# Kernel optimization log

Hardware: AMD Instinct MI355X
Metric: run time of the kernel (lower is better)

The kernel has to match this reference:

```python
import jax, jax.numpy as jnp
import numpy as np

WS = (17, 5, 1)
NT = 23  # 17+5+1 tokens across levels
TABLE_ROWS = (2 * WS[0] - 1) * (2 * WS[0] - 1)  # 1089


def _rel_index():
    cs = []
    for i, w in enumerate(WS):
        c = np.arange(w, dtype=np.float32) - w // 2
        if i < len(WS) - 1:
            c = c * WS[0] / w  # rescale coarser levels to finest grid
        cs.append(c)
    c = np.concatenate(cs)  # [23]
    return (c[:, None] - c[None, :]) + (WS[0] - 1)  # [23,23] float

REL_IDX = jnp.asarray(_rel_index())


def _avgpool1d(x):
    # AvgPool1d(kernel=2, stride=2, padding=1, count_include_pad=False) on last axis (odd L)
    return jnp.concatenate([x[..., :1], (x[..., 1::2] + x[..., 2::2]) * 0.5], axis=-1)


def _l2norm(x):
    n = jnp.linalg.norm(x, axis=-1, keepdims=True)
    return x / jnp.maximum(n, 1e-12)


def _pos_embed(table, abs_bias):
    # table [1089,H], abs_bias [3,H,1,1,1] -> [1,H,1,23,23]
    idx = REL_IDX.reshape(-1)
    fl = jnp.clip(jnp.floor(idx), 0, TABLE_ROWS - 1).astype(jnp.int32)
    ce = jnp.clip(jnp.ceil(idx), 0, TABLE_ROWS - 1).astype(jnp.int32)
    w_ce = (idx - fl.astype(idx.dtype))[:, None]
    pe = (1.0 - w_ce) * table[fl] + w_ce * table[ce]  # [529,H]
    H = table.shape[1]
    pe = pe.reshape(1, 1, NT, NT, H).transpose(0, 4, 1, 2, 3)  # [1,H,1,23,23]
    chunks = jnp.split(pe, [WS[0], WS[0] + WS[1]], axis=3)
    chunks = [c + abs_bias[i][None] for i, c in enumerate(chunks)]
    return jnp.concatenate(chunks, axis=-2)


def _hifi(xh0, xh1, xh2, h_table, h_abs, h_proj_w, h_proj_b):
    q = jnp.concatenate([xh0[0], xh1[0], xh2[0]], axis=-2)  # [B,Hh,hd,23,S]
    k = jnp.concatenate([xh0[1], xh1[1], xh2[1]], axis=-2)
    v = jnp.concatenate([xh0[2], xh1[2], xh2[2]], axis=-2)
    attn = jnp.einsum('bhdts,bhdus->bhdtu', _l2norm(q), _l2norm(k))
    attn = attn + _pos_embed(h_table, h_abs)
    attn = jax.nn.softmax(attn, axis=-1)
    out = jnp.einsum('bhdtu,bhdus->bhdts', attn, v)
    return out @ h_proj_w.T + h_proj_b


def _lofi(xl0, xl1, xl2, l_table, l_abs, l_proj_w, l_proj_b):
    q = jnp.concatenate([xl0[0], xl1[0], xl2[0]], axis=-2)  # [B,Hl,hd,23,S]
    kvs = []
    for i, x in enumerate((xl0, xl1, xl2)):
        kv = x[1:]  # [2,B,Hl,hd,t_i,S]
        if i != 2:  # pool token axis for the two finer levels
            kv = jnp.moveaxis(_avgpool1d(jnp.moveaxis(kv, -2, -1)), -1, -2)
        kvs.append(kv)
    kv = jnp.concatenate(kvs, axis=-2)  # [2,B,Hl,hd,13,S]
    k, v = kv[0], kv[1]
    attn = jnp.einsum('bhdts,bhdus->bhdtu', _l2norm(q), _l2norm(k))  # [B,Hl,hd,23,13]
    pe = _pos_embed(l_table, l_abs)  # [1,Hl,1,23,23]
    Hl = l_table.shape[1]
    p1 = _avgpool1d(pe[..., :WS[0]].reshape(Hl, NT, WS[0])).reshape(1, Hl, 1, NT, -1)
    p2 = _avgpool1d(pe[..., WS[0]:WS[0] + WS[1]].reshape(Hl, NT, WS[1])).reshape(1, Hl, 1, NT, -1)
    p3 = pe[..., -1:]
    attn = attn + jnp.concatenate([p1, p2, p3], axis=-1)
    attn = jax.nn.softmax(attn, axis=-1)
    out = jnp.einsum('bhdtu,bhdus->bhdts', attn, v)
    return out @ l_proj_w.T + l_proj_b


def _forward(xh0, xh1, xh2, xl0, xl1, xl2, h_table, h_abs, l_table, l_abs,
             h_proj_w, h_proj_b, l_proj_w, l_proj_b):
    h_out = _hifi(xh0, xh1, xh2, h_table, h_abs, h_proj_w, h_proj_b)  # [B,1,64,23,S]
    l_out = _lofi(xl0, xl1, xl2, l_table, l_abs, l_proj_w, l_proj_b)  # [B,3,64,23,S]
    return jnp.concatenate([h_out, l_out], axis=1)  # [B,4,64,23,S]


def setup_inputs() -> dict:
    key = jax.random.key(0)
    ks = jax.random.split(key, 14)
    B, hd, S = 4, 64, 1024
    Hh, Hl = 1, 3
    d = {
        'xh0': jax.random.normal(ks[0], (3, B, Hh, hd, 17, S), jnp.float32),
        'xh1': jax.random.normal(ks[1], (3, B, Hh, hd, 5, S), jnp.float32),
        'xh2': jax.random.normal(ks[2], (3, B, Hh, hd, 1, S), jnp.float32),
        'xl0': jax.random.normal(ks[3], (3, B, Hl, hd, 17, S), jnp.float32),
        'xl1': jax.random.normal(ks[4], (3, B, Hl, hd, 5, S), jnp.float32),
        'xl2': jax.random.normal(ks[5], (3, B, Hl, hd, 1, S), jnp.float32),
        'h_table': jax.random.normal(ks[6], (TABLE_ROWS, Hh), jnp.float32) * 0.02,
        'h_abs': jax.random.normal(ks[7], (3, Hh, 1, 1, 1), jnp.float32) * 0.02,
        'l_table': jax.random.normal(ks[8], (TABLE_ROWS, Hl), jnp.float32) * 0.02,
        'l_abs': jax.random.normal(ks[9], (3, Hl, 1, 1, 1), jnp.float32) * 0.02,
        'h_proj_w': jax.random.normal(ks[10], (S, S), jnp.float32) / np.sqrt(S),
        'h_proj_b': jax.random.normal(ks[11], (S,), jnp.float32) * 0.01,
        'l_proj_w': jax.random.normal(ks[12], (S, S), jnp.float32) / np.sqrt(S),
        'l_proj_b': jax.random.normal(ks[13], (S,), jnp.float32) * 0.01,
    }
    return d


def reference(xh0, xh1, xh2, xl0, xl1, xl2, h_table, h_abs, l_table, l_abs,
              h_proj_w, h_proj_b, l_proj_w, l_proj_b):
    return _forward(xh0, xh1, xh2, xl0, xl1, xl2, h_table, h_abs, l_table, l_abs,
                    h_proj_w, h_proj_b, l_proj_w, l_proj_b)
```

## Files before the change

### kernel.cpp

```cpp
#include <hip/hip_runtime.h>
#include <hip/hip_bf16.h>
#include <stdint.h>

#define DEV __device__ __forceinline__

typedef float f32x4 __attribute__((ext_vector_type(4)));
typedef __bf16 bf16x8 __attribute__((ext_vector_type(8)));

DEV __bf16 tobf(float x){
  union { __hip_bfloat16 s; __bf16 b; } u; u.s = __float2bfloat16(x); return u.b;
}
DEV float bflo(uint32_t u){ return __uint_as_float(u << 16); }
DEV float bfhi(uint32_t u){ return __uint_as_float(u & 0xffff0000u); }
DEV float dot4(const float4& a, const float4& b){
  return a.x*b.x + a.y*b.y + a.z*b.z + a.w*b.w;
}
DEV bf16x8 pack8(const float4& a, const float4& b){
  bf16x8 r;
  r[0]=tobf(a.x); r[1]=tobf(a.y); r[2]=tobf(a.z); r[3]=tobf(a.w);
  r[4]=tobf(b.x); r[5]=tobf(b.y); r[6]=tobf(b.z); r[7]=tobf(b.w);
  return r;
}
DEV uint32_t f2bf2(float x, float y){
  union { __hip_bfloat16 b[2]; uint32_t u; } cv;
  cv.b[0] = __float2bfloat16(x); cv.b[1] = __float2bfloat16(y);
  return cv.u;
}

DEV float relc(int j){
  if (j < 17) return (float)(j - 8);
  if (j < 22) return (float)(j - 19) * 3.4f;
  return 0.0f;
}
DEV int band_of(int t){ return t < 17 ? 0 : (t < 22 ? 1 : 2); }

template<int MODE> DEV void pool_map(int u, int& a, int& b){
  if (MODE == 0){ a = u; b = u; return; }
  if (u == 0){ a = 0; b = 0; }
  else if (u < 9){ a = 2*u - 1; b = 2*u; }
  else if (u == 9){ a = 17; b = 17; }
  else if (u < 12){ a = 2*u - 2; b = 2*u - 1; }
  else { a = 22; b = 22; }
}

DEV float interp_tab(const float* tab, int H, int h, int t, int u){
  float idx = relc(t) - relc(u) + 16.0f;
  float fl = floorf(idx);
  float ce = ceilf(idx);
  int fi = (int)fminf(fmaxf(fl, 0.f), 1088.f);
  int ci = (int)fminf(fmaxf(ce, 0.f), 1088.f);
  float w = idx - fl;
  return (1.0f - w) * tab[fi*H + h] + w * tab[ci*H + h];
}

__global__ __launch_bounds__(256) void prep_kernel(
    const float* __restrict__ htab, const float* __restrict__ habs,
    const float* __restrict__ ltab, const float* __restrict__ labs,
    const float* __restrict__ hw, const float* __restrict__ lw,
    float* __restrict__ pe_h, float* __restrict__ pe_l,
    __hip_bfloat16* __restrict__ whb, __hip_bfloat16* __restrict__ wlb)
{
  int bid = blockIdx.x, tid = threadIdx.x;
  if (bid < 1024){
    int i = (bid*256 + tid)*8;
    const float* src; __hip_bfloat16* dst;
    if (i < 1048576){ src = hw + i; dst = whb + i; }
    else { src = lw + (i - 1048576); dst = wlb + (i - 1048576); }
    float4 x0 = *(const float4*)(src);
    float4 x1 = *(const float4*)(src + 4);
    uint4 o;
    o.x = f2bf2(x0.x, x0.y); o.y = f2bf2(x0.z, x0.w);
    o.z = f2bf2(x1.x, x1.y); o.w = f2bf2(x1.z, x1.w);
    *(uint4*)dst = o;
  } else if (bid == 1024){
    for (int j = tid; j < 529; j += 256){
      int t = j / 23, u = j % 23;
      pe_h[j] = interp_tab(htab, 1, 0, t, u) + habs[band_of(t)];
    }
  } else {
    for (int j = tid; j < 897; j += 256){
      int h = j / 299, r = j % 299, t = r / 13, u = r % 13;
      int a, b; pool_map<1>(u, a, b);
      pe_l[j] = 0.5f * (interp_tab(ltab, 3, h, t, a) + interp_tab(ltab, 3, h, t, b))
              + labs[band_of(t)*3 + h];
    }
  }
}

template<int MODE>
DEV void qk_group(int gm, int hh,
    const float* __restrict__ x0, const float* __restrict__ x1, const float* __restrict__ x2,
    float* __restrict__ SpB,
    float* Spart , float* qnp , float* knp )
{
  constexpr int U = (MODE == 0) ? 23 : 13;
  constexpr int H = (MODE == 0) ? 1 : 3;
  int b, h, d;
  if (MODE == 0){ b = gm >> 6; h = 0; d = gm & 63; }
  else { b = gm / 192; int r = gm % 192; h = r >> 6; d = r & 63; }

  const int tid  = threadIdx.x;
  const int lane = tid & 63;
  const int w    = tid >> 6;
  const int lrow = lane & 15;
  const int kq   = lane >> 4;

  auto base_of = [&](int sel, int band) -> const float* {
    if (band == 0) return x0 + (size_t)((((sel*4 + b)*H + h)*64 + d)*17) * 1024;
    if (band == 1) return x1 + (size_t)((((sel*4 + b)*H + h)*64 + d)*5) * 1024;
    return x2 + (size_t)(((sel*4 + b)*H + h)*64 + d) * 1024;
  };
  const float* qb0 = base_of(0,0); const float* qb1 = base_of(0,1); const float* qb2 = base_of(0,2);
  const float* kb0 = base_of(1,0); const float* kb1 = base_of(1,1); const float* kb2 = base_of(1,2);

  auto rowp = [&](const float* r0, const float* r1, const float* r2, int t) -> const float* {
    if (t < 17) return r0 + (size_t)t * 1024;
    if (t < 22) return r1 + (size_t)(t - 17) * 1024;
    return r2;
  };

  const float* qr[2]; bool qv[2];
  #pragma unroll
  for (int mi = 0; mi < 2; ++mi){
    int t = mi*16 + lrow;
    qv[mi] = (t < 23);
    qr[mi] = qv[mi] ? rowp(qb0,qb1,qb2,t) : qb0;
  }
  const float* krA[2]; const float* krB[2]; bool kv[2];
  #pragma unroll
  for (int ni = 0; ni < 2; ++ni){
    int u = ni*16 + lrow;
    kv[ni] = (u < U);
    int au, bu; pool_map<MODE>(kv[ni] ? u : 0, au, bu);
    krA[ni] = rowp(kb0,kb1,kb2,au);
    krB[ni] = rowp(kb0,kb1,kb2,bu);
  }

  f32x4 acc[2][2] = {};
  float qss[2] = {0.f, 0.f}, kss[2] = {0.f, 0.f};
  const int sbase = hh*512 + w*128 + kq*8;

  #pragma unroll 2
  for (int kk = 0; kk < 4; ++kk){
    const int s = sbase + kk*32;
    bf16x8 qf[2], kf[2];
    #pragma unroll
    for (int mi = 0; mi < 2; ++mi){
      float4 v0 = {0,0,0,0}, v1 = {0,0,0,0};
      if (qv[mi]){
        v0 = *(const float4*)(qr[mi] + s);
        v1 = *(const float4*)(qr[mi] + s + 4);
      }
      qss[mi] += dot4(v0,v0) + dot4(v1,v1);
      qf[mi] = pack8(v0, v1);
    }
    #pragma unroll
    for (int ni = 0; ni < 2; ++ni){
      float4 v0 = {0,0,0,0}, v1 = {0,0,0,0};
      if ((MODE == 0 || ni == 0) && kv[ni]){
        if (MODE == 0){
          v0 = *(const float4*)(krA[ni] + s);
          v1 = *(const float4*)(krA[ni] + s + 4);
        } else {
          float4 a0 = *(const float4*)(krA[ni] + s);
          float4 a1 = *(const float4*)(krA[ni] + s + 4);
          float4 b0 = *(const float4*)(krB[ni] + s);
          float4 b1 = *(const float4*)(krB[ni] + s + 4);
          v0.x = 0.5f*(a0.x+b0.x); v0.y = 0.5f*(a0.y+b0.y); v0.z = 0.5f*(a0.z+b0.z); v0.w = 0.5f*(a0.w+b0.w);
          v1.x = 0.5f*(a1.x+b1.x); v1.y = 0.5f*(a1.y+b1.y); v1.z = 0.5f*(a1.z+b1.z); v1.w = 0.5f*(a1.w+b1.w);
        }
      }
      kss[ni] += dot4(v0,v0) + dot4(v1,v1);
      kf[ni] = pack8(v0, v1);
    }
    #pragma unroll
    for (int mi = 0; mi < 2; ++mi){
      #pragma unroll
      for (int ni = 0; ni < 2; ++ni){
        if (MODE == 0 || ni == 0)
          acc[mi][ni] = __builtin_amdgcn_mfma_f32_16x16x32_bf16(qf[mi], kf[ni], acc[mi][ni], 0, 0, 0);
      }
    }
  }

  #pragma unroll
  for (int i = 0; i < 2; ++i){
    qss[i] += __shfl_xor(qss[i], 16); qss[i] += __shfl_xor(qss[i], 32);
    kss[i] += __shfl_xor(kss[i], 16); kss[i] += __shfl_xor(kss[i], 32);
  }
  if (lane < 16){
    qnp[w*32 + lane]      = qss[0];
    qnp[w*32 + 16 + lane] = qss[1];
    knp[w*32 + lane]      = kss[0];
    knp[w*32 + 16 + lane] = kss[1];
  }
  #pragma unroll
  for (int mi = 0; mi < 2; ++mi)
    #pragma unroll
    for (int ni = 0; ni < 2; ++ni)
      #pragma unroll
      for (int j = 0; j < 4; ++j)
        Spart[w*1056 + (mi*16 + kq*4 + j)*33 + ni*16 + lrow] = acc[mi][ni][j];
  __syncthreads();

  if (tid < 32){
    SpB[1024 + tid] = qnp[tid] + qnp[32+tid] + qnp[64+tid] + qnp[96+tid];
  } else if (tid < 64){
    int c = tid - 32;
    SpB[1056 + c] = knp[c] + knp[32+c] + knp[64+c] + knp[96+c];
  }
  {
    int r  = tid >> 3;
    int c0 = (tid & 7) * 4;
    float4 o;
    o.x = Spart[r*33+c0+0] + Spart[1056+r*33+c0+0] + Spart[2112+r*33+c0+0] + Spart[3168+r*33+c0+0];
    o.y = Spart[r*33+c0+1] + Spart[1056+r*33+c0+1] + Spart[2112+r*33+c0+1] + Spart[3168+r*33+c0+1];
    o.z = Spart[r*33+c0+2] + Spart[1056+r*33+c0+2] + Spart[2112+r*33+c0+2] + Spart[3168+r*33+c0+2];
    o.w = Spart[r*33+c0+3] + Spart[1056+r*33+c0+3] + Spart[2112+r*33+c0+3] + Spart[3168+r*33+c0+3];
    *(float4*)(SpB + r*32 + c0) = o;
  }
}

__global__ __launch_bounds__(256) void qkv_kernel(
    const float* __restrict__ xh0, const float* __restrict__ xh1, const float* __restrict__ xh2,
    const float* __restrict__ xl0, const float* __restrict__ xl1, const float* __restrict__ xl2,
    float* __restrict__ Sp, __hip_bfloat16* __restrict__ Vb)
{
  __shared__ __align__(16) float Spart[4*32*33];
  __shared__ float qnp[4*32], knp[4*32];
  const int bid = blockIdx.x;
  const int tid = threadIdx.x;

  if (bid < 992){
    auto vsrc = [&](int r, const float*& pa, const float*& pb){
      if (r < 5888){
        int g = r / 23, u = r - g*23;
        int b = g >> 6, d = g & 63;
        const float* v0 = xh0 + (size_t)(((8 + b)*64 + d)*17) * 1024;
        const float* v1 = xh1 + (size_t)(((8 + b)*64 + d)*5) * 1024;
        const float* v2 = xh2 + (size_t)((8 + b)*64 + d) * 1024;
        pa = (u < 17) ? v0 + (size_t)u*1024 : (u < 22 ? v1 + (size_t)(u-17)*1024 : v2);
        pb = pa;
      } else {
        int rr = r - 5888;
        int gm = rr / 13, u = rr - gm*13;
        int b = gm / 192, rem = gm % 192, h = rem >> 6, d = rem & 63;
        const float* v0 = xl0 + (size_t)((((8 + b)*3 + h)*64 + d)*17) * 1024;
        const float* v1 = xl1 + (size_t)((((8 + b)*3 + h)*64 + d)*5) * 1024;
        const float* v2 = xl2 + (size_t)(((8 + b)*3 + h)*64 + d) * 1024;
        int au, bu; pool_map<1>(u, au, bu);
        pa = (au < 17) ? v0 + (size_t)au*1024 : (au < 22 ? v1 + (size_t)(au-17)*1024 : v2);
        pb = (bu < 17) ? v0 + (size_t)bu*1024 : (bu < 22 ? v1 + (size_t)(bu-17)*1024 : v2);
      }
    };
    const int r0 = bid * 16;
    const int c0 = tid * 4;
    #pragma unroll 4
    for (int i = 0; i < 16; ++i){
      int r = r0 + i;
      const float *pa, *pb; vsrc(r, pa, pb);
      float4 a = *(const float4*)(pa + c0);
      if (pb != pa){
        float4 c = *(const float4*)(pb + c0);
        a.x = 0.5f*(a.x + c.x); a.y = 0.5f*(a.y + c.y);
        a.z = 0.5f*(a.z + c.z); a.w = 0.5f*(a.w + c.w);
      }
      uint2 o; o.x = f2bf2(a.x, a.y); o.y = f2bf2(a.z, a.w);
      *(uint2*)(Vb + (size_t)r*1024 + c0) = o;
    }
    return;
  }

  const int qb = bid - 992;
  const int g = qb >> 1, hh = qb & 1;
  float* SpB = Sp + (size_t)qb * 1088;
  if (g < 256) qk_group<0>(g, hh, xh0, xh1, xh2, SpB, Spart, qnp, knp);
  else         qk_group<1>(g - 256, hh, xl0, xl1, xl2, SpB, Spart, qnp, knp);
}

__global__ __launch_bounds__(256) void gemm_vw(
    const __hip_bfloat16* __restrict__ A,
    const __hip_bfloat16* __restrict__ Wh, const __hip_bfloat16* __restrict__ Wl,
    __hip_bfloat16* __restrict__ VW)
{
  __shared__ __hip_bfloat16 lA[2][128*64];
  __shared__ __hip_bfloat16 lB[2][128*64];
  const int tid  = threadIdx.x;
  const int lane = tid & 63;

  const int bid = blockIdx.x;
  const int swz = (bid & 7) * 124 + (bid >> 3);
  const int mt = swz >> 3, nt = swz & 7;
  const int tM = mt * 128, tN = nt * 128;
  const bool hifi = (mt < 46);
  const __hip_bfloat16* W = hifi ? Wh : Wl;

  const int wm = ((tid >> 6) >> 1) * 64, wn = ((tid >> 6) & 1) * 64;
  f32x4 acc[4][4] = {};

  const int srow = tid >> 3;
  const int scol = ((tid & 7) * 8) ^ ((srow & 7) * 8);
  const __hip_bfloat16* ga = A + (size_t)(tM + srow) * 1024 + scol;
  const __hip_bfloat16* gb = W + (size_t)(tN + srow) * 1024 + scol;

  auto stage = [&](int buf, int k0){
    #pragma unroll
    for (int q = 0; q < 4; ++q){
      __builtin_amdgcn_global_load_lds(
        (const __attribute__((address_space(1))) void*)(ga + k0 + (size_t)q*32*1024),
        (__attribute__((address_space(3))) void*)(&lA[buf][q*2048 + tid*8]), 16, 0, 0);
      __builtin_amdgcn_global_load_lds(
        (const __attribute__((address_space(1))) void*)(gb + k0 + (size_t)q*32*1024),
        (__attribute__((address_space(3))) void*)(&lB[buf][q*2048 + tid*8]), 16, 0, 0);
    }
  };

  const int rsw = (lane & 7) * 8;
  auto compute = [&](int buf){
    #pragma unroll
    for (int kk = 0; kk < 2; ++kk){
      const int cb = (kk*32 + (lane >> 4)*8) ^ rsw;
      bf16x8 af[4], bfr[4];
      #pragma unroll
      for (int mi = 0; mi < 4; ++mi)
        af[mi] = *(const bf16x8*)(&lA[buf][(wm + mi*16 + (lane & 15))*64 + cb]);
      #pragma unroll
      for (int ni = 0; ni < 4; ++ni)
        bfr[ni] = *(const bf16x8*)(&lB[buf][(wn + ni*16 + (lane & 15))*64 + cb]);
      #pragma unroll
      for (int mi = 0; mi < 4; ++mi){
        #pragma unroll
        for (int ni = 0; ni < 4; ++ni)
          acc[mi][ni] = __builtin_amdgcn_mfma_f32_16x16x32_bf16(af[mi], bfr[ni], acc[mi][ni], 0, 0, 0);
      }
    }
  };

  stage(0, 0);
  __syncthreads();
  int cur = 0;
  #pragma unroll 1
  for (int t = 0; t < 15; ++t){
    stage(cur ^ 1, (t + 1) * 64);
    compute(cur);
    __syncthreads();
    cur ^= 1;
  }
  compute(cur);

  #pragma unroll
  for (int mi = 0; mi < 4; ++mi){
    #pragma unroll
    for (int j = 0; j < 4; ++j){
      int r = tM + wm + mi*16 + (lane >> 4)*4 + j;
      __hip_bfloat16* po = VW + (size_t)r * 1024 + tN + wn + (lane & 15);
      #pragma unroll
      for (int ni = 0; ni < 4; ++ni)
        po[ni*16] = __float2bfloat16(acc[mi][ni][j]);
    }
  }
}

template<int MODE>
DEV void mix_group(int g, int sh, int tid,
    const float* __restrict__ Sp, const float* __restrict__ pe,
    const __hip_bfloat16* __restrict__ VW, const float* __restrict__ bias,
    float* __restrict__ out, float* lds_p)
{
  constexpr int U  = (MODE == 0) ? 23 : 13;
  constexpr int UP = (MODE == 0) ? 24 : 16;
  int gm = (MODE == 0) ? g : g - 256;
  int b, h, d;
  if (MODE == 0){ b = gm >> 6; h = 0; d = gm & 63; }
  else { b = gm / 192; int rem = gm % 192; h = rem >> 6; d = rem & 63; }

  {
    int r = tid >> 3, c0 = (tid & 7) * 4;
    const float* A = Sp + (size_t)(2*g) * 1088;
    const float* B = A + 1088;
    float qn = A[1024 + r] + B[1024 + r];
    float iqn = 1.0f / fmaxf(sqrtf(qn), 1e-12f);
    float vals[4];
    #pragma unroll
    for (int j = 0; j < 4; ++j){
      int c = c0 + j;
      bool valid = (r < 23) && (c < U);
      if (valid){
        float sv = A[r*32 + c] + B[r*32 + c];
        float kn = A[1056 + c] + B[1056 + c];
        float ikn = 1.0f / fmaxf(sqrtf(kn), 1e-12f);
        float pv = (MODE == 0) ? pe[r*23 + c] : pe[(h*23 + r)*13 + c];
        vals[j] = sv * iqn * ikn + pv;
      } else vals[j] = -3.0e38f;
    }
    float m = fmaxf(fmaxf(vals[0], vals[1]), fmaxf(vals[2], vals[3]));
    m = fmaxf(m, __shfl_xor(m, 1)); m = fmaxf(m, __shfl_xor(m, 2)); m = fmaxf(m, __shfl_xor(m, 4));
    float e[4], ssum = 0.f;
    #pragma unroll
    for (int j = 0; j < 4; ++j){ e[j] = __expf(vals[j] - m); ssum += e[j]; }
    ssum += __shfl_xor(ssum, 1); ssum += __shfl_xor(ssum, 2); ssum += __shfl_xor(ssum, 4);
    float inv = 1.0f / ssum;
    if (r < 23){
      #pragma unroll
      for (int j = 0; j < 4; ++j)
        lds_p[r*32 + c0 + j] = (c0 + j < U) ? e[j] * inv : 0.f;
    }
  }
  __syncthreads();

  const int s0 = sh*512 + tid*2;
  const uint16_t* vwb = (const uint16_t*)VW +
      ((MODE == 0) ? (size_t)g*23*1024 : (size_t)(5888 + gm*13)*1024) + s0;
  float2 vv[UP];
  #pragma unroll
  for (int u = 0; u < UP; ++u){
    if (u < U){
      uint32_t w2 = *(const uint32_t*)(vwb + (size_t)u*1024);
      vv[u].x = bflo(w2); vv[u].y = bfhi(w2);
    } else { vv[u].x = 0.f; vv[u].y = 0.f; }
  }
  const float bx = bias[s0], by = bias[s0 + 1];
  const int orow0 = (MODE == 0) ? (b*5888 + d*23) : (b*5888 + (1 + h)*1472 + d*23);

  #pragma unroll 2
  for (int t = 0; t < 23; ++t){
    float ax = bx, ay = by;
    #pragma unroll
    for (int u4 = 0; u4 < UP/4; ++u4){
      float4 p = *(const float4*)(lds_p + t*32 + u4*4);
      ax += p.x*vv[u4*4+0].x + p.y*vv[u4*4+1].x + p.z*vv[u4*4+2].x + p.w*vv[u4*4+3].x;
      ay += p.x*vv[u4*4+0].y + p.y*vv[u4*4+1].y + p.z*vv[u4*4+2].y + p.w*vv[u4*4+3].y;
    }
    float2 o2; o2.x = ax; o2.y = ay;
    *(float2*)(out + (size_t)(orow0 + t)*1024 + s0) = o2;
  }
}

__global__ __launch_bounds__(256) void mix_all(
    const float* __restrict__ Sp, const float* __restrict__ pe_h, const float* __restrict__ pe_l,
    const __hip_bfloat16* __restrict__ VW,
    const float* __restrict__ hb, const float* __restrict__ lb,
    float* __restrict__ out)
{
  __shared__ __align__(16) float lds_p[23*32];
  int bid = blockIdx.x;
  int g = bid >> 1, sh = bid & 1;
  if (g < 256) mix_group<0>(g, sh, threadIdx.x, Sp, pe_h, VW, hb, out, lds_p);
  else         mix_group<1>(g, sh, threadIdx.x, Sp, pe_l, VW, lb, out, lds_p);
}

extern "C" void kernel_launch(void* const* d_in, const int* in_sizes, int n_in,
                              void* d_out, int out_size, void* d_ws, size_t ws_size,
                              hipStream_t stream) {
  const float* xh0  = (const float*)d_in[0];
  const float* xh1  = (const float*)d_in[1];
  const float* xh2  = (const float*)d_in[2];
  const float* xl0  = (const float*)d_in[3];
  const float* xl1  = (const float*)d_in[4];
  const float* xl2  = (const float*)d_in[5];
  const float* htab = (const float*)d_in[6];
  const float* habs = (const float*)d_in[7];
  const float* ltab = (const float*)d_in[8];
  const float* labs = (const float*)d_in[9];
  const float* hw   = (const float*)d_in[10];
  const float* hb   = (const float*)d_in[11];
  const float* lw   = (const float*)d_in[12];
  const float* lb   = (const float*)d_in[13];
  float* out = (float*)d_out;

  char* ws = (char*)d_ws;
  float* pe_h = (float*)ws;
  float* pe_l = (float*)(ws + 2176);
  __hip_bfloat16* whb = (__hip_bfloat16*)(ws + 8192);
  __hip_bfloat16* wlb = (__hip_bfloat16*)(ws + 8192 + 2097152);
  __hip_bfloat16* VW  = (__hip_bfloat16*)(ws + 8192 + 4194304);
  float* Sp           = (float*)(ws + 8192 + 4194304 + 32505856);

  __hip_bfloat16* Vb = (__hip_bfloat16*)out;

  prep_kernel<<<1026, 256, 0, stream>>>(htab, habs, ltab, labs, hw, lw, pe_h, pe_l, whb, wlb);
  qkv_kernel<<<3040, 256, 0, stream>>>(xh0, xh1, xh2, xl0, xl1, xl2, Sp, Vb);
  gemm_vw<<<992, 256, 0, stream>>>(Vb, whb, wlb, VW);
  mix_all<<<2048, 256, 0, stream>>>(Sp, pe_h, pe_l, VW, hb, lb, out);
}
```

Measured before the change: 159.2 us.

## Stage Q/K rows into LDS asynchronously and merge V conversion into QK blocks

The QK blocks now copy all 23 Q and 23 K rows for their half of S into XOR-swizzled shared memory with global_load_lds. The pooled K rows are then read from LDS, so each source row is fetched once instead of being reloaded by several lanes. The separate V-conversion blocks are removed: every block converts 8 V rows, issuing those loads before the async stage and storing them after it so the two overlap. The grid shrinks from 3040 to 2048 blocks, but each block now uses about 94 KB of LDS, which lowers occupancy.

```diff
diff --git a/kernel.cpp b/kernel.cpp
--- a/kernel.cpp
+++ b/kernel.cpp
@@ -25,6 +25,10 @@
   union { __hip_bfloat16 b[2]; uint32_t u; } cv;
   cv.b[0] = __float2bfloat16(x); cv.b[1] = __float2bfloat16(y);
   return cv.u;
+}
+DEV float4 avg4(const float4& a, const float4& b){
+  float4 r; r.x=0.5f*(a.x+b.x); r.y=0.5f*(a.y+b.y); r.z=0.5f*(a.z+b.z); r.w=0.5f*(a.w+b.w);
+  return r;
 }
 
 DEV float relc(int j){
@@ -88,22 +92,17 @@
 }
 
 template<int MODE>
-DEV void qk_group(int gm, int hh,
+DEV void qk_stage(int gm, int hh,
     const float* __restrict__ x0, const float* __restrict__ x1, const float* __restrict__ x2,
-    float* __restrict__ SpB,
-    float* Spart , float* qnp , float* knp )
-{
-  constexpr int U = (MODE == 0) ? 23 : 13;
+    float* Qs, float* Ks)
+{
   constexpr int H = (MODE == 0) ? 1 : 3;
   int b, h, d;
   if (MODE == 0){ b = gm >> 6; h = 0; d = gm & 63; }
   else { b = gm / 192; int r = gm % 192; h = r >> 6; d = r & 63; }
-
   const int tid  = threadIdx.x;
   const int lane = tid & 63;
   const int w    = tid >> 6;
-  const int lrow = lane & 15;
-  const int kq   = lane >> 4;
 
   auto base_of = [&](int sel, int band) -> const float* {
     if (band == 0) return x0 + (size_t)((((sel*4 + b)*H + h)*64 + d)*17) * 1024;
@@ -112,62 +111,72 @@
   };
   const float* qb0 = base_of(0,0); const float* qb1 = base_of(0,1); const float* qb2 = base_of(0,2);
   const float* kb0 = base_of(1,0); const float* kb1 = base_of(1,1); const float* kb2 = base_of(1,2);
-
   auto rowp = [&](const float* r0, const float* r1, const float* r2, int t) -> const float* {
     if (t < 17) return r0 + (size_t)t * 1024;
     if (t < 22) return r1 + (size_t)(t - 17) * 1024;
     return r2;
   };
 
-  const float* qr[2]; bool qv[2];
-  #pragma unroll
-  for (int mi = 0; mi < 2; ++mi){
-    int t = mi*16 + lrow;
-    qv[mi] = (t < 23);
-    qr[mi] = qv[mi] ? rowp(qb0,qb1,qb2,t) : qb0;
-  }
-  const float* krA[2]; const float* krB[2]; bool kv[2];
-  #pragma unroll
-  for (int ni = 0; ni < 2; ++ni){
-    int u = ni*16 + lrow;
-    kv[ni] = (u < U);
-    int au, bu; pool_map<MODE>(kv[ni] ? u : 0, au, bu);
-    krA[ni] = rowp(kb0,kb1,kb2,au);
-    krB[ni] = rowp(kb0,kb1,kb2,bu);
-  }
+  for (int c = w; c < 46; c += 4){
+    const int isK = (c >= 23);
+    const int t = isK ? c - 23 : c;
+    const float* src = (isK ? rowp(kb0,kb1,kb2,t) : rowp(qb0,qb1,qb2,t))
+                       + hh*512 + ((lane ^ (t & 7)) << 2);
+    float* dst = (isK ? Ks : Qs) + t*512 + (lane << 2);
+    __builtin_amdgcn_global_load_lds(
+        (const __attribute__((address_space(1))) void*)src,
+        (__attribute__((address_space(3))) void*)dst, 16, 0, 0);
+    __builtin_amdgcn_global_load_lds(
+        (const __attribute__((address_space(1))) void*)(src + 256),
+        (__attribute__((address_space(3))) void*)(dst + 256), 16, 0, 0);
+  }
+}
+
+template<int MODE>
+DEV void qk_compute(float* __restrict__ SpB,
+    const float* Qs, const float* Ks,
+    float* Spart , float* qnp , float* knp )
+{
+  constexpr int U = (MODE == 0) ? 23 : 13;
+  const int tid  = threadIdx.x;
+  const int lane = tid & 63;
+  const int w    = tid >> 6;
+  const int lrow = lane & 15;
+  const int kq   = lane >> 4;
+
+  auto ld = [&](const float* B, int t, int s) -> float4 {
+    int u = s >> 2;
+    return *(const float4*)(B + t*512 + ((u ^ (t & 7)) << 2));
+  };
 
   f32x4 acc[2][2] = {};
   float qss[2] = {0.f, 0.f}, kss[2] = {0.f, 0.f};
-  const int sbase = hh*512 + w*128 + kq*8;
-
-  #pragma unroll 2
+  const int sbase = w*128 + kq*8;
+
+  #pragma unroll
   for (int kk = 0; kk < 4; ++kk){
     const int s = sbase + kk*32;
     bf16x8 qf[2], kf[2];
     #pragma unroll
     for (int mi = 0; mi < 2; ++mi){
+      int t = mi*16 + lrow;
       float4 v0 = {0,0,0,0}, v1 = {0,0,0,0};
-      if (qv[mi]){
-        v0 = *(const float4*)(qr[mi] + s);
-        v1 = *(const float4*)(qr[mi] + s + 4);
-      }
+      if (t < 23){ v0 = ld(Qs, t, s); v1 = ld(Qs, t, s + 4); }
       qss[mi] += dot4(v0,v0) + dot4(v1,v1);
       qf[mi] = pack8(v0, v1);
     }
     #pragma unroll
     for (int ni = 0; ni < 2; ++ni){
+      int u2 = ni*16 + lrow;
       float4 v0 = {0,0,0,0}, v1 = {0,0,0,0};
-      if ((MODE == 0 || ni == 0) && kv[ni]){
-        if (MODE == 0){
-          v0 = *(const float4*)(krA[ni] + s);
-          v1 = *(const float4*)(krA[ni] + s + 4);
-        } else {
-          float4 a0 = *(const float4*)(krA[ni] + s);
-          float4 a1 = *(const float4*)(krA[ni] + s + 4);
-          float4 b0 = *(const float4*)(krB[ni] + s);
-          float4 b1 = *(const float4*)(krB[ni] + s + 4);
-          v0.x = 0.5f*(a0.x+b0.x); v0.y = 0.5f*(a0.y+b0.y); v0.z = 0.5f*(a0.z+b0.z); v0.w = 0.5f*(a0.w+b0.w);
-          v1.x = 0.5f*(a1.x+b1.x); v1.y = 0.5f*(a1.y+b1.y); v1.z = 0.5f*(a1.z+b1.z); v1.w = 0.5f*(a1.w+b1.w);
+      if (MODE == 0){
+        if (u2 < 23){ v0 = ld(Ks, u2, s); v1 = ld(Ks, u2, s + 4); }
+      } else if (ni == 0){
+        if (u2 < 13){
+          int au, bu; pool_map<1>(u2, au, bu);
+          float4 a0 = ld(Ks, au, s), a1 = ld(Ks, au, s + 4);
+          float4 b0 = ld(Ks, bu, s), b1 = ld(Ks, bu, s + 4);
+          v0 = avg4(a0, b0); v1 = avg4(a1, b1);
         }
       }
       kss[ni] += dot4(v0,v0) + dot4(v1,v1);
@@ -226,56 +235,70 @@
     const float* __restrict__ xl0, const float* __restrict__ xl1, const float* __restrict__ xl2,
     float* __restrict__ Sp, __hip_bfloat16* __restrict__ Vb)
 {
+  __shared__ __align__(16) float Qs[23*512];
+  __shared__ __align__(16) float Ks[23*512];
   __shared__ __align__(16) float Spart[4*32*33];
   __shared__ float qnp[4*32], knp[4*32];
+
   const int bid = blockIdx.x;
   const int tid = threadIdx.x;
-
-  if (bid < 992){
-    auto vsrc = [&](int r, const float*& pa, const float*& pb){
-      if (r < 5888){
-        int g = r / 23, u = r - g*23;
-        int b = g >> 6, d = g & 63;
-        const float* v0 = xh0 + (size_t)(((8 + b)*64 + d)*17) * 1024;
-        const float* v1 = xh1 + (size_t)(((8 + b)*64 + d)*5) * 1024;
-        const float* v2 = xh2 + (size_t)((8 + b)*64 + d) * 1024;
-        pa = (u < 17) ? v0 + (size_t)u*1024 : (u < 22 ? v1 + (size_t)(u-17)*1024 : v2);
-        pb = pa;
-      } else {
-        int rr = r - 5888;
-        int gm = rr / 13, u = rr - gm*13;
-        int b = gm / 192, rem = gm % 192, h = rem >> 6, d = rem & 63;
-        const float* v0 = xl0 + (size_t)((((8 + b)*3 + h)*64 + d)*17) * 1024;
-        const float* v1 = xl1 + (size_t)((((8 + b)*3 + h)*64 + d)*5) * 1024;
-        const float* v2 = xl2 + (size_t)(((8 + b)*3 + h)*64 + d) * 1024;
-        int au, bu; pool_map<1>(u, au, bu);
-        pa = (au < 17) ? v0 + (size_t)au*1024 : (au < 22 ? v1 + (size_t)(au-17)*1024 : v2);
-        pb = (bu < 17) ? v0 + (size_t)bu*1024 : (bu < 22 ? v1 + (size_t)(bu-17)*1024 : v2);
-      }
-    };
-    const int r0 = bid * 16;
-    const int c0 = tid * 4;
-    #pragma unroll 4
-    for (int i = 0; i < 16; ++i){
-      int r = r0 + i;
+  const int g = bid >> 1, hh = bid & 1;
+
+  auto vsrc = [&](int r, const float*& pa, const float*& pb){
+    if (r < 5888){
+      int gg = r / 23, u = r - gg*23;
+      int b = gg >> 6, d = gg & 63;
+      const float* v0 = xh0 + (size_t)(((8 + b)*64 + d)*17) * 1024;
+      const float* v1 = xh1 + (size_t)(((8 + b)*64 + d)*5) * 1024;
+      const float* v2 = xh2 + (size_t)((8 + b)*64 + d) * 1024;
+      pa = (u < 17) ? v0 + (size_t)u*1024 : (u < 22 ? v1 + (size_t)(u-17)*1024 : v2);
+      pb = pa;
+    } else {
+      int rr = r - 5888;
+      int gm = rr / 13, u = rr - gm*13;
+      int b = gm / 192, rem = gm % 192, h = rem >> 6, d = rem & 63;
+      const float* v0 = xl0 + (size_t)((((8 + b)*3 + h)*64 + d)*17) * 1024;
+      const float* v1 = xl1 + (size_t)((((8 + b)*3 + h)*64 + d)*5) * 1024;
+      const float* v2 = xl2 + (size_t)(((8 + b)*3 + h)*64 + d) * 1024;
+      int au, bu; pool_map<1>(u, au, bu);
+      pa = (au < 17) ? v0 + (size_t)au*1024 : (au < 22 ? v1 + (size_t)(au-17)*1024 : v2);
+      pb = (bu < 17) ? v0 + (size_t)bu*1024 : (bu < 22 ? v1 + (size_t)(bu-17)*1024 : v2);
+    }
+  };
+  const int c0v = tid * 4;
+  float4 va[8], vb[8];
+  bool two[8], ok[8];
+  #pragma unroll
+  for (int i = 0; i < 8; ++i){
+    int r = bid*8 + i;
+    ok[i] = (r < 15872);
+    two[i] = false;
+    if (ok[i]){
       const float *pa, *pb; vsrc(r, pa, pb);
-      float4 a = *(const float4*)(pa + c0);
-      if (pb != pa){
-        float4 c = *(const float4*)(pb + c0);
-        a.x = 0.5f*(a.x + c.x); a.y = 0.5f*(a.y + c.y);
-        a.z = 0.5f*(a.z + c.z); a.w = 0.5f*(a.w + c.w);
-      }
+      va[i] = *(const float4*)(pa + c0v);
+      two[i] = (pb != pa);
+      if (two[i]) vb[i] = *(const float4*)(pb + c0v);
+    }
+  }
+
+  if (g < 256) qk_stage<0>(g,       hh, xh0, xh1, xh2, Qs, Ks);
+  else         qk_stage<1>(g - 256, hh, xl0, xl1, xl2, Qs, Ks);
+
+  #pragma unroll
+  for (int i = 0; i < 8; ++i){
+    if (ok[i]){
+      float4 a = va[i];
+      if (two[i]) a = avg4(a, vb[i]);
       uint2 o; o.x = f2bf2(a.x, a.y); o.y = f2bf2(a.z, a.w);
-      *(uint2*)(Vb + (size_t)r*1024 + c0) = o;
-    }
-    return;
-  }
-
-  const int qb = bid - 992;
-  const int g = qb >> 1, hh = qb & 1;
-  float* SpB = Sp + (size_t)qb * 1088;
-  if (g < 256) qk_group<0>(g, hh, xh0, xh1, xh2, SpB, Spart, qnp, knp);
-  else         qk_group<1>(g - 256, hh, xl0, xl1, xl2, SpB, Spart, qnp, knp);
+      *(uint2*)(Vb + (size_t)(bid*8 + i)*1024 + c0v) = o;
+    }
+  }
+
+  __syncthreads();
+
+  float* SpB = Sp + (size_t)bid * 1088;
+  if (g < 256) qk_compute<0>(SpB, Qs, Ks, Spart, qnp, knp);
+  else         qk_compute<1>(SpB, Qs, Ks, Spart, qnp, knp);
 }
 
 __global__ __launch_bounds__(256) void gemm_vw(
@@ -479,7 +502,7 @@
   __hip_bfloat16* Vb = (__hip_bfloat16*)out;
 
   prep_kernel<<<1026, 256, 0, stream>>>(htab, habs, ltab, labs, hw, lw, pe_h, pe_l, whb, wlb);
-  qkv_kernel<<<3040, 256, 0, stream>>>(xh0, xh1, xh2, xl0, xl1, xl2, Sp, Vb);
+  qkv_kernel<<<2048, 256, 0, stream>>>(xh0, xh1, xh2, xl0, xl1, xl2, Sp, Vb);
   gemm_vw<<<992, 256, 0, stream>>>(Vb, whb, wlb, VW);
   mix_all<<<2048, 256, 0, stream>>>(Sp, pe_h, pe_l, VW, hb, lb, out);
 }
```

Result: slower. 172.0 us (+8.0%).

## Split V conversion into own kernel and quarter-split QK reduction across blocks

Applied to the files above, without the earlier changes.

Moves the V fp32-to-bf16 conversion (with token pooling) out of the fused qkv kernel into a separate vconv kernel that loads eight rows per block with all loads issued up front. The QK partial-score kernel now splits the 1024-wide reduction into four quarters instead of two, doubling block count for more parallelism, and the mix kernel sums four partials. The bf16 weight copies are relocated into spare space in the output buffer. This adds one kernel launch, more partial-sum traffic through Sp, and risks the output-aliasing staying correct.

```diff
diff --git a/kernel.cpp b/kernel.cpp
--- a/kernel.cpp
+++ b/kernel.cpp
@@ -25,6 +25,10 @@
   union { __hip_bfloat16 b[2]; uint32_t u; } cv;
   cv.b[0] = __float2bfloat16(x); cv.b[1] = __float2bfloat16(y);
   return cv.u;
+}
+DEV float4 avg4(const float4& a, const float4& b){
+  float4 r; r.x=0.5f*(a.x+b.x); r.y=0.5f*(a.y+b.y); r.z=0.5f*(a.z+b.z); r.w=0.5f*(a.w+b.w);
+  return r;
 }
 
 DEV float relc(int j){
@@ -87,8 +91,54 @@
   }
 }
 
+__global__ __launch_bounds__(256) void vconv_kernel(
+    const float* __restrict__ xh0, const float* __restrict__ xh1, const float* __restrict__ xh2,
+    const float* __restrict__ xl0, const float* __restrict__ xl1, const float* __restrict__ xl2,
+    __hip_bfloat16* __restrict__ Vb)
+{
+  const int bid = blockIdx.x, tid = threadIdx.x;
+  auto vsrc = [&](int r, const float*& pa, const float*& pb){
+    if (r < 5888){
+      int gg = r / 23, u = r - gg*23;
+      int b = gg >> 6, d = gg & 63;
+      const float* v0 = xh0 + (size_t)(((8 + b)*64 + d)*17) * 1024;
+      const float* v1 = xh1 + (size_t)(((8 + b)*64 + d)*5) * 1024;
+      const float* v2 = xh2 + (size_t)((8 + b)*64 + d) * 1024;
+      pa = (u < 17) ? v0 + (size_t)u*1024 : (u < 22 ? v1 + (size_t)(u-17)*1024 : v2);
+      pb = pa;
+    } else {
+      int rr = r - 5888;
+      int gm = rr / 13, u = rr - gm*13;
+      int b = gm / 192, rem = gm % 192, h = rem >> 6, d = rem & 63;
+      const float* v0 = xl0 + (size_t)((((8 + b)*3 + h)*64 + d)*17) * 1024;
+      const float* v1 = xl1 + (size_t)((((8 + b)*3 + h)*64 + d)*5) * 1024;
+      const float* v2 = xl2 + (size_t)(((8 + b)*3 + h)*64 + d) * 1024;
+      int au, bu; pool_map<1>(u, au, bu);
+      pa = (au < 17) ? v0 + (size_t)au*1024 : (au < 22 ? v1 + (size_t)(au-17)*1024 : v2);
+      pb = (bu < 17) ? v0 + (size_t)bu*1024 : (bu < 22 ? v1 + (size_t)(bu-17)*1024 : v2);
+    }
+  };
+  const int c0 = tid * 4;
+  float4 va[8], vb[8]; bool two[8];
+  #pragma unroll
+  for (int i = 0; i < 8; ++i){
+    int r = bid*8 + i;
+    const float *pa, *pb; vsrc(r, pa, pb);
+    va[i] = *(const float4*)(pa + c0);
+    two[i] = (pb != pa);
+    if (two[i]) vb[i] = *(const float4*)(pb + c0);
+  }
+  #pragma unroll
+  for (int i = 0; i < 8; ++i){
+    float4 a = va[i];
+    if (two[i]) a = avg4(a, vb[i]);
+    uint2 o; o.x = f2bf2(a.x, a.y); o.y = f2bf2(a.z, a.w);
+    *(uint2*)(Vb + (size_t)(bid*8 + i)*1024 + c0) = o;
+  }
+}
+
 template<int MODE>
-DEV void qk_group(int gm, int hh,
+DEV void qk_group(int gm, int qt,
     const float* __restrict__ x0, const float* __restrict__ x1, const float* __restrict__ x2,
     float* __restrict__ SpB,
     float* Spart , float* qnp , float* knp )
@@ -138,10 +188,10 @@
 
   f32x4 acc[2][2] = {};
   float qss[2] = {0.f, 0.f}, kss[2] = {0.f, 0.f};
-  const int sbase = hh*512 + w*128 + kq*8;
-
-  #pragma unroll 2
-  for (int kk = 0; kk < 4; ++kk){
+  const int sbase = qt*256 + w*64 + kq*8;
+
+  #pragma unroll
+  for (int kk = 0; kk < 2; ++kk){
     const int s = sbase + kk*32;
     bf16x8 qf[2], kf[2];
     #pragma unroll
@@ -166,8 +216,7 @@
           float4 a1 = *(const float4*)(krA[ni] + s + 4);
           float4 b0 = *(const float4*)(krB[ni] + s);
           float4 b1 = *(const float4*)(krB[ni] + s + 4);
-          v0.x = 0.5f*(a0.x+b0.x); v0.y = 0.5f*(a0.y+b0.y); v0.z = 0.5f*(a0.z+b0.z); v0.w = 0.5f*(a0.w+b0.w);
-          v1.x = 0.5f*(a1.x+b1.x); v1.y = 0.5f*(a1.y+b1.y); v1.z = 0.5f*(a1.z+b1.z); v1.w = 0.5f*(a1.w+b1.w);
+          v0 = avg4(a0, b0); v1 = avg4(a1, b1);
         }
       }
       kss[ni] += dot4(v0,v0) + dot4(v1,v1);
@@ -221,61 +270,18 @@
   }
 }
 
-__global__ __launch_bounds__(256) void qkv_kernel(
+__global__ __launch_bounds__(256) void qk4_kernel(
     const float* __restrict__ xh0, const float* __restrict__ xh1, const float* __restrict__ xh2,
     const float* __restrict__ xl0, const float* __restrict__ xl1, const float* __restrict__ xl2,
-    float* __restrict__ Sp, __hip_bfloat16* __restrict__ Vb)
+    float* __restrict__ Sp)
 {
   __shared__ __align__(16) float Spart[4*32*33];
   __shared__ float qnp[4*32], knp[4*32];
-  const int bid = blockIdx.x;
-  const int tid = threadIdx.x;
-
-  if (bid < 992){
-    auto vsrc = [&](int r, const float*& pa, const float*& pb){
-      if (r < 5888){
-        int g = r / 23, u = r - g*23;
-        int b = g >> 6, d = g & 63;
-        const float* v0 = xh0 + (size_t)(((8 + b)*64 + d)*17) * 1024;
-        const float* v1 = xh1 + (size_t)(((8 + b)*64 + d)*5) * 1024;
-        const float* v2 = xh2 + (size_t)((8 + b)*64 + d) * 1024;
-        pa = (u < 17) ? v0 + (size_t)u*1024 : (u < 22 ? v1 + (size_t)(u-17)*1024 : v2);
-        pb = pa;
-      } else {
-        int rr = r - 5888;
-        int gm = rr / 13, u = rr - gm*13;
-        int b = gm / 192, rem = gm % 192, h = rem >> 6, d = rem & 63;
-        const float* v0 = xl0 + (size_t)((((8 + b)*3 + h)*64 + d)*17) * 1024;
-        const float* v1 = xl1 + (size_t)((((8 + b)*3 + h)*64 + d)*5) * 1024;
-        const float* v2 = xl2 + (size_t)(((8 + b)*3 + h)*64 + d) * 1024;
-        int au, bu; pool_map<1>(u, au, bu);
-        pa = (au < 17) ? v0 + (size_t)au*1024 : (au < 22 ? v1 + (size_t)(au-17)*1024 : v2);
-        pb = (bu < 17) ? v0 + (size_t)bu*1024 : (bu < 22 ? v1 + (size_t)(bu-17)*1024 : v2);
-      }
-    };
-    const int r0 = bid * 16;
-    const int c0 = tid * 4;
-    #pragma unroll 4
-    for (int i = 0; i < 16; ++i){
-      int r = r0 + i;
-      const float *pa, *pb; vsrc(r, pa, pb);
-      float4 a = *(const float4*)(pa + c0);
-      if (pb != pa){
-        float4 c = *(const float4*)(pb + c0);
-        a.x = 0.5f*(a.x + c.x); a.y = 0.5f*(a.y + c.y);
-        a.z = 0.5f*(a.z + c.z); a.w = 0.5f*(a.w + c.w);
-      }
-      uint2 o; o.x = f2bf2(a.x, a.y); o.y = f2bf2(a.z, a.w);
-      *(uint2*)(Vb + (size_t)r*1024 + c0) = o;
-    }
-    return;
-  }
-
-  const int qb = bid - 992;
-  const int g = qb >> 1, hh = qb & 1;
-  float* SpB = Sp + (size_t)qb * 1088;
-  if (g < 256) qk_group<0>(g, hh, xh0, xh1, xh2, SpB, Spart, qnp, knp);
-  else         qk_group<1>(g - 256, hh, xl0, xl1, xl2, SpB, Spart, qnp, knp);
+  int bid = blockIdx.x;
+  int g = bid >> 2, qt = bid & 3;
+  float* SpB = Sp + (size_t)bid * 1088;
+  if (g < 256) qk_group<0>(g,       qt, xh0, xh1, xh2, SpB, Spart, qnp, knp);
+  else         qk_group<1>(g - 256, qt, xl0, xl1, xl2, SpB, Spart, qnp, knp);
 }
 
 __global__ __launch_bounds__(256) void gemm_vw(
@@ -376,9 +382,11 @@
 
   {
     int r = tid >> 3, c0 = (tid & 7) * 4;
-    const float* A = Sp + (size_t)(2*g) * 1088;
-    const float* B = A + 1088;
-    float qn = A[1024 + r] + B[1024 + r];
+    const float* A0 = Sp + (size_t)(4*g) * 1088;
+    const float* A1 = A0 + 1088;
+    const float* A2 = A0 + 2176;
+    const float* A3 = A0 + 3264;
+    float qn = A0[1024 + r] + A1[1024 + r] + A2[1024 + r] + A3[1024 + r];
     float iqn = 1.0f / fmaxf(sqrtf(qn), 1e-12f);
     float vals[4];
     #pragma unroll
@@ -386,8 +394,8 @@
       int c = c0 + j;
       bool valid = (r < 23) && (c < U);
       if (valid){
-        float sv = A[r*32 + c] + B[r*32 + c];
-        float kn = A[1056 + c] + B[1056 + c];
+        float sv = A0[r*32 + c] + A1[r*32 + c] + A2[r*32 + c] + A3[r*32 + c];
+        float kn = A0[1056 + c] + A1[1056 + c] + A2[1056 + c] + A3[1056 + c];
         float ikn = 1.0f / fmaxf(sqrtf(kn), 1e-12f);
         float pv = (MODE == 0) ? pe[r*23 + c] : pe[(h*23 + r)*13 + c];
         vals[j] = sv * iqn * ikn + pv;
@@ -471,15 +479,16 @@
   char* ws = (char*)d_ws;
   float* pe_h = (float*)ws;
   float* pe_l = (float*)(ws + 2176);
-  __hip_bfloat16* whb = (__hip_bfloat16*)(ws + 8192);
-  __hip_bfloat16* wlb = (__hip_bfloat16*)(ws + 8192 + 2097152);
-  __hip_bfloat16* VW  = (__hip_bfloat16*)(ws + 8192 + 4194304);
-  float* Sp           = (float*)(ws + 8192 + 4194304 + 32505856);
-
-  __hip_bfloat16* Vb = (__hip_bfloat16*)out;
+  __hip_bfloat16* VW  = (__hip_bfloat16*)(ws + 8192);
+  float* Sp           = (float*)(ws + 8192 + 32505856);
+
+  __hip_bfloat16* Vb  = (__hip_bfloat16*)out;
+  __hip_bfloat16* whb = (__hip_bfloat16*)(out + 23068672);
+  __hip_bfloat16* wlb = whb + 1048576;
 
   prep_kernel<<<1026, 256, 0, stream>>>(htab, habs, ltab, labs, hw, lw, pe_h, pe_l, whb, wlb);
-  qkv_kernel<<<3040, 256, 0, stream>>>(xh0, xh1, xh2, xl0, xl1, xl2, Sp, Vb);
+  vconv_kernel<<<1984, 256, 0, stream>>>(xh0, xh1, xh2, xl0, xl1, xl2, Vb);
+  qk4_kernel<<<4096, 256, 0, stream>>>(xh0, xh1, xh2, xl0, xl1, xl2, Sp);
   gemm_vw<<<992, 256, 0, stream>>>(Vb, whb, wlb, VW);
   mix_all<<<2048, 256, 0, stream>>>(Sp, pe_h, pe_l, VW, hb, lb, out);
 }
```

New measurement: 164.2 us. 1.03x slower.
